# Kernel optimization log

Hardware: AMD Instinct MI355X
Metric: run time of the kernel (lower is better)

## Reference

```python
import jax, jax.numpy as jnp
import numpy as np

B, N, C, W = 128, 512, 128, 128
MASK_FILL = -1e-06  # faithful to original (sic: -1e-06, not -1e6)


def setup_inputs() -> dict:
    key = jax.random.key(0)
    ks = jax.random.split(key, 8)
    s = 1.0 / np.sqrt(C)
    return {
        "x": jax.random.normal(ks[0], (B, N, C), dtype=jnp.float32),
        "Wq": jax.random.normal(ks[1], (C, W), dtype=jnp.float32) * s,
        "bq": jnp.zeros((W,), dtype=jnp.float32),
        "Wk": jax.random.normal(ks[2], (C, W), dtype=jnp.float32) * s,
        "bk": jnp.zeros((W,), dtype=jnp.float32),
        "Wv": jax.random.normal(ks[3], (C, W), dtype=jnp.float32) * s,
        "bv": jnp.zeros((W,), dtype=jnp.float32),
        "valid_len": jax.random.randint(ks[4], (B,), 0, N, dtype=jnp.int64),
    }


def reference(x, Wq, bq, Wk, bk, Wv, bv, valid_len):
    # QKV projections: [B, N, W]
    q = jnp.einsum("bnc,cw->bnw", x, Wq) + bq
    k = jnp.einsum("bnc,cw->bnw", x, Wk) + bk
    v = jnp.einsum("bnc,cw->bnw", x, Wv) + bv
    # scores: [B, N, N]
    scores = jnp.einsum("bnw,bmw->bnm", q, k)
    # masked softmax: positions m where m > valid_len[b] get MASK_FILL
    # (mask is identical across query rows n since valid_len is per-batch)
    keep = jnp.arange(N)[None, None, :] <= valid_len[:, None, None]  # [B,1,N]
    scores = jnp.where(keep, scores, MASK_FILL)
    attn = jax.nn.softmax(scores, axis=-1)
    return jnp.einsum("bnm,bmw->bnw", attn, v)
```

## Files before the change

### kernel.cpp

```cpp
#include <hip/hip_runtime.h>
#include <hip/hip_fp16.h>

#define B_ 128
#define N_ 512
#define C_ 128
#define W_ 128
#define LDSW 136

typedef _Float16 f16;
typedef _Float16 f16x8 __attribute__((ext_vector_type(8)));
typedef _Float16 f16x4 __attribute__((ext_vector_type(4)));
typedef float f32x4 __attribute__((ext_vector_type(4)));

#define MFMA16(a, b, c) __builtin_amdgcn_mfma_f32_16x16x32_f16(a, b, c, 0, 0, 0)

__global__ __launch_bounds__(256) void prep_w(const float* __restrict__ Wq,
                                              const float* __restrict__ Wk,
                                              const float* __restrict__ Wv,
                                              f16* __restrict__ wT) {
  const float* src = blockIdx.x == 0 ? Wq : (blockIdx.x == 1 ? Wk : Wv);
  f16* dst = wT + (size_t)blockIdx.x * C_ * W_;
  const int t = threadIdx.x;
  for (int i = 0; i < 64; ++i) {
    int idx = t + 256 * i;
    int w = idx >> 7, c = idx & 127;
    dst[idx] = (f16)src[c * W_ + w];
  }
}

__global__ __launch_bounds__(256) void proj(const float* __restrict__ x,
                                            const float* __restrict__ bq,
                                            const float* __restrict__ bk,
                                            const float* __restrict__ bv,
                                            const f16* __restrict__ wT,
                                            f16* __restrict__ q,
                                            f16* __restrict__ k,
                                            f16* __restrict__ vT) {
  __shared__ f16 xs[128 * LDSW];
  __shared__ f16 wls[128 * LDSW];
  const int b = blockIdx.y, n0 = blockIdx.x * 128;
  const int t = threadIdx.x, wave = t >> 6, lane = t & 63;
  const int quad = lane >> 4, l15 = lane & 15;

  for (int i = 0; i < 16; ++i) {
    int idx = t + 256 * i;
    int row = idx >> 5, c4 = idx & 31;
    const float4 v = *reinterpret_cast<const float4*>(
        x + ((size_t)(b * N_ + n0 + row)) * C_ + c4 * 4);
    f16x4 h;
    h.x = (f16)v.x; h.y = (f16)v.y; h.z = (f16)v.z; h.w = (f16)v.w;
    *reinterpret_cast<f16x4*>(&xs[row * LDSW + c4 * 4]) = h;
  }
  __syncthreads();

  f16x8 af[2][4];
  for (int mt = 0; mt < 2; ++mt)
    for (int ks = 0; ks < 4; ++ks)
      af[mt][ks] = *reinterpret_cast<const f16x8*>(
          &xs[(wave * 32 + mt * 16 + l15) * LDSW + ks * 32 + quad * 8]);

  for (int ph = 0; ph < 3; ++ph) {
    __syncthreads();
    for (int i = 0; i < 8; ++i) {
      int idx = t + 256 * i;
      int row = idx >> 4, c16 = idx & 15;
      *reinterpret_cast<f16x8*>(&wls[row * LDSW + c16 * 8]) =
          *reinterpret_cast<const f16x8*>(wT + (size_t)ph * 16384 + idx * 8);
    }
    __syncthreads();

    f32x4 acc[2][8];
    for (int mt = 0; mt < 2; ++mt)
      for (int ct = 0; ct < 8; ++ct) acc[mt][ct] = {0.f, 0.f, 0.f, 0.f};

    for (int ct = 0; ct < 8; ++ct)
      for (int ks = 0; ks < 4; ++ks) {
        f16x8 bf = *reinterpret_cast<const f16x8*>(
            &wls[(ct * 16 + l15) * LDSW + ks * 32 + quad * 8]);
        acc[0][ct] = MFMA16(af[0][ks], bf, acc[0][ct]);
        acc[1][ct] = MFMA16(af[1][ks], bf, acc[1][ct]);
      }

    const float* bias = ph == 0 ? bq : (ph == 1 ? bk : bv);
    if (ph < 2) {
      f16* dst = ph == 0 ? q : k;
      for (int mt = 0; mt < 2; ++mt)
        for (int ct = 0; ct < 8; ++ct) {
          int wcol = ct * 16 + l15;
          float bb = bias[wcol];
          for (int r = 0; r < 4; ++r) {
            int n = n0 + wave * 32 + mt * 16 + quad * 4 + r;
            dst[((size_t)(b * N_ + n)) * W_ + wcol] = (f16)(acc[mt][ct][r] + bb);
          }
        }
    } else {
      for (int mt = 0; mt < 2; ++mt)
        for (int ct = 0; ct < 8; ++ct) {
          int wcol = ct * 16 + l15;
          float bb = bias[wcol];
          int n = n0 + wave * 32 + mt * 16 + quad * 4;
          f16x4 h;
          h.x = (f16)(acc[mt][ct][0] + bb);
          h.y = (f16)(acc[mt][ct][1] + bb);
          h.z = (f16)(acc[mt][ct][2] + bb);
          h.w = (f16)(acc[mt][ct][3] + bb);
          *reinterpret_cast<f16x4*>(&vT[((size_t)(b * W_ + wcol)) * N_ + n]) = h;
        }
    }
  }
}

__global__ __launch_bounds__(256, 2) void flash(const f16* __restrict__ q,
                                                const f16* __restrict__ k,
                                                const f16* __restrict__ vT,
                                                const int* __restrict__ vlen,
                                                float* __restrict__ out) {
  __shared__ f16 qls[128 * LDSW];
  __shared__ f16 pls[128 * LDSW];
  const int b = blockIdx.x, m0 = blockIdx.y * 128;
  const int t = threadIdx.x, wave = t >> 6, lane = t & 63;
  const int quad = lane >> 4, l15 = lane & 15;
  const int vl = vlen[b];

  for (int i = 0; i < 8; ++i) {
    int idx = t + 256 * i;
    int row = idx >> 4, c16 = idx & 15;
    *reinterpret_cast<f16x8*>(&qls[row * LDSW + c16 * 8]) =
        *reinterpret_cast<const f16x8*>(
            q + ((size_t)(b * N_ + m0 + row)) * W_ + c16 * 8);
  }
  __syncthreads();

  f32x4 oacc[2][8];
  for (int mt = 0; mt < 2; ++mt)
    for (int ct = 0; ct < 8; ++ct) oacc[mt][ct] = {0.f, 0.f, 0.f, 0.f};
  float mrun[8], lrun[8];
  for (int ct = 0; ct < 8; ++ct) { mrun[ct] = -3.4e38f; lrun[ct] = 0.f; }

  for (int j = 0; j < 4; ++j) {
    const int n0 = j * 128;

    f16x8 kf[2][4];
    for (int mt = 0; mt < 2; ++mt)
      for (int kt = 0; kt < 4; ++kt)
        kf[mt][kt] = *reinterpret_cast<const f16x8*>(
            k + ((size_t)(b * N_ + n0 + wave * 32 + mt * 16 + l15)) * W_ +
            kt * 32 + quad * 8);

    f32x4 sacc[2][8];
    for (int mt = 0; mt < 2; ++mt)
      for (int ct = 0; ct < 8; ++ct) sacc[mt][ct] = {0.f, 0.f, 0.f, 0.f};
    for (int ct = 0; ct < 8; ++ct)
      for (int kt = 0; kt < 4; ++kt) {
        f16x8 bf = *reinterpret_cast<const f16x8*>(
            &qls[(ct * 16 + l15) * LDSW + kt * 32 + quad * 8]);
        sacc[0][ct] = MFMA16(kf[0][kt], bf, sacc[0][ct]);
        sacc[1][ct] = MFMA16(kf[1][kt], bf, sacc[1][ct]);
      }

    for (int mt = 0; mt < 2; ++mt)
      for (int r = 0; r < 4; ++r) {
        int n = n0 + wave * 32 + mt * 16 + quad * 4 + r;
        if (n > vl)
          for (int ct = 0; ct < 8; ++ct) sacc[mt][ct][r] = -1e-6f;
      }

    float cm[8];
    for (int ct = 0; ct < 8; ++ct) {
      float c0 = fmaxf(fmaxf(sacc[0][ct][0], sacc[0][ct][1]),
                       fmaxf(sacc[0][ct][2], sacc[0][ct][3]));
      float c1 = fmaxf(fmaxf(sacc[1][ct][0], sacc[1][ct][1]),
                       fmaxf(sacc[1][ct][2], sacc[1][ct][3]));
      float c = fmaxf(c0, c1);
      c = fmaxf(c, __shfl_xor(c, 16));
      c = fmaxf(c, __shfl_xor(c, 32));
      cm[ct] = c;
    }
    __shared__ float redbuf[4 * 128];
    __syncthreads();
    if (quad == 0)
      for (int ct = 0; ct < 8; ++ct) redbuf[wave * 128 + ct * 16 + l15] = cm[ct];
    __syncthreads();
    float alpha[8];
    for (int ct = 0; ct < 8; ++ct) {
      int mcol = ct * 16 + l15;
      float c = fmaxf(fmaxf(redbuf[mcol], redbuf[128 + mcol]),
                      fmaxf(redbuf[256 + mcol], redbuf[384 + mcol]));
      float mnew = fmaxf(mrun[ct], c);
      alpha[ct] = __expf(mrun[ct] - mnew);
      mrun[ct] = mnew;
    }
    float ls[8];
    for (int ct = 0; ct < 8; ++ct) {
      float s = 0.f;
      for (int mt = 0; mt < 2; ++mt)
        for (int r = 0; r < 4; ++r) {
          float p = __expf(sacc[mt][ct][r] - mrun[ct]);
          sacc[mt][ct][r] = p;
          s += p;
        }
      s += __shfl_xor(s, 16);
      s += __shfl_xor(s, 32);
      ls[ct] = s;
    }
    if (quad == 0)
      for (int ct = 0; ct < 8; ++ct) redbuf[wave * 128 + ct * 16 + l15] = ls[ct];
    for (int mt = 0; mt < 2; ++mt)
      for (int ct = 0; ct < 8; ++ct) {
        f16x4 h;
        h.x = (f16)sacc[mt][ct][0];
        h.y = (f16)sacc[mt][ct][1];
        h.z = (f16)sacc[mt][ct][2];
        h.w = (f16)sacc[mt][ct][3];
        *reinterpret_cast<f16x4*>(
            &pls[(ct * 16 + l15) * LDSW + wave * 32 + mt * 16 + quad * 4]) = h;
      }
    f16x8 vf[2][4];
    for (int mt = 0; mt < 2; ++mt)
      for (int kt = 0; kt < 4; ++kt)
        vf[mt][kt] = *reinterpret_cast<const f16x8*>(
            vT + ((size_t)(b * W_ + wave * 32 + mt * 16 + l15)) * N_ + n0 +
            kt * 32 + quad * 8);
    __syncthreads();
    for (int ct = 0; ct < 8; ++ct) {
      int mcol = ct * 16 + l15;
      float s = redbuf[mcol] + redbuf[128 + mcol] + redbuf[256 + mcol] +
                redbuf[384 + mcol];
      lrun[ct] = lrun[ct] * alpha[ct] + s;
      oacc[0][ct] *= alpha[ct];
      oacc[1][ct] *= alpha[ct];
    }
    for (int ct = 0; ct < 8; ++ct)
      for (int kt = 0; kt < 4; ++kt) {
        f16x8 bf = *reinterpret_cast<const f16x8*>(
            &pls[(ct * 16 + l15) * LDSW + kt * 32 + quad * 8]);
        oacc[0][ct] = MFMA16(vf[0][kt], bf, oacc[0][ct]);
        oacc[1][ct] = MFMA16(vf[1][kt], bf, oacc[1][ct]);
      }
  }

  for (int ct = 0; ct < 8; ++ct) {
    float inv = 1.f / lrun[ct];
    int m = m0 + ct * 16 + l15;
    for (int mt = 0; mt < 2; ++mt) {
      int w = wave * 32 + mt * 16 + quad * 4;
      float4 o;
      o.x = oacc[mt][ct][0] * inv;
      o.y = oacc[mt][ct][1] * inv;
      o.z = oacc[mt][ct][2] * inv;
      o.w = oacc[mt][ct][3] * inv;
      *reinterpret_cast<float4*>(&out[((size_t)(b * N_ + m)) * W_ + w]) = o;
    }
  }
}

extern "C" void kernel_launch(void* const* d_in, const int* in_sizes, int n_in,
                              void* d_out, int out_size, void* d_ws,
                              size_t ws_size, hipStream_t stream) {
  const float* x  = (const float*)d_in[0];
  const float* Wq = (const float*)d_in[1];
  const float* bq = (const float*)d_in[2];
  const float* Wk = (const float*)d_in[3];
  const float* bk = (const float*)d_in[4];
  const float* Wv = (const float*)d_in[5];
  const float* bv = (const float*)d_in[6];
  const int* vlen = (const int*)d_in[7];
  float* out = (float*)d_out;

  char* ws = (char*)d_ws;
  f16* wT = (f16*)ws;
  f16* q  = (f16*)(ws + (1u << 20));
  f16* k  = (f16*)(ws + (1u << 20) + (16u << 20));
  f16* vT = (f16*)(ws + (1u << 20) + (32u << 20));

  prep_w<<<3, 256, 0, stream>>>(Wq, Wk, Wv, wT);
  proj<<<dim3(4, 128), 256, 0, stream>>>(x, bq, bk, bv, wT, q, k, vT);
  flash<<<dim3(128, 4), 256, 0, stream>>>(q, k, vT, vlen, out);
}
```

Before: 146.3 us.

## Give each wave its own query rows in flash to drop cross-wave softmax reductions

The flash kernel is restructured so each wave owns 32 query rows and covers all 128 keys per tile. Row max and row sum then reduce within the wave, which removes the shared-memory reduction buffer and most block-wide barriers. Q fragments stay in registers instead of LDS. Each wave now loads the whole K and V tile directly from global memory, so redundant global/L2 traffic goes up four times. Q is also pre-scaled by log2(e) in the projection so exp2f can replace __expf, and the weight transpose in prep_w now goes through LDS to get coalesced reads.

After: 172.5 us. 17.8% more time.

```diff
diff --git a/kernel.cpp b/kernel.cpp
--- a/kernel.cpp
+++ b/kernel.cpp
@@ -1,5 +1,6 @@
 #include <hip/hip_runtime.h>
 #include <hip/hip_fp16.h>
+#include <math.h>
 
 #define B_ 128
 #define N_ 512
@@ -14,17 +15,31 @@
 
 #define MFMA16(a, b, c) __builtin_amdgcn_mfma_f32_16x16x32_f16(a, b, c, 0, 0, 0)
 
+#define LOG2E 1.44269504f
+#define MASKF (-1e-6f * LOG2E)
+
 __global__ __launch_bounds__(256) void prep_w(const float* __restrict__ Wq,
                                               const float* __restrict__ Wk,
                                               const float* __restrict__ Wv,
                                               f16* __restrict__ wT) {
+  __shared__ float xs[128 * 129];
   const float* src = blockIdx.x == 0 ? Wq : (blockIdx.x == 1 ? Wk : Wv);
   f16* dst = wT + (size_t)blockIdx.x * C_ * W_;
   const int t = threadIdx.x;
+  for (int i = 0; i < 16; ++i) {
+    int idx = t + 256 * i;
+    int c = idx >> 5, w4 = idx & 31;
+    float4 v = *reinterpret_cast<const float4*>(src + c * W_ + w4 * 4);
+    xs[c * 129 + w4 * 4 + 0] = v.x;
+    xs[c * 129 + w4 * 4 + 1] = v.y;
+    xs[c * 129 + w4 * 4 + 2] = v.z;
+    xs[c * 129 + w4 * 4 + 3] = v.w;
+  }
+  __syncthreads();
   for (int i = 0; i < 64; ++i) {
     int idx = t + 256 * i;
     int w = idx >> 7, c = idx & 127;
-    dst[idx] = (f16)src[c * W_ + w];
+    dst[idx] = (f16)xs[c * 129 + w];
   }
 }
 
@@ -81,8 +96,9 @@
         acc[1][ct] = MFMA16(af[1][ks], bf, acc[1][ct]);
       }
 
-    const float* bias = ph == 0 ? bq : (ph == 1 ? bk : bv);
     if (ph < 2) {
+      const float* bias = ph == 0 ? bq : bk;
+      const float scale = ph == 0 ? LOG2E : 1.0f;
       f16* dst = ph == 0 ? q : k;
       for (int mt = 0; mt < 2; ++mt)
         for (int ct = 0; ct < 8; ++ct) {
@@ -90,14 +106,15 @@
           float bb = bias[wcol];
           for (int r = 0; r < 4; ++r) {
             int n = n0 + wave * 32 + mt * 16 + quad * 4 + r;
-            dst[((size_t)(b * N_ + n)) * W_ + wcol] = (f16)(acc[mt][ct][r] + bb);
+            dst[((size_t)(b * N_ + n)) * W_ + wcol] =
+                (f16)((acc[mt][ct][r] + bb) * scale);
           }
         }
     } else {
       for (int mt = 0; mt < 2; ++mt)
         for (int ct = 0; ct < 8; ++ct) {
           int wcol = ct * 16 + l15;
-          float bb = bias[wcol];
+          float bb = bv[wcol];
           int n = n0 + wave * 32 + mt * 16 + quad * 4;
           f16x4 h;
           h.x = (f16)(acc[mt][ct][0] + bb);
@@ -115,140 +132,118 @@
                                                 const f16* __restrict__ vT,
                                                 const int* __restrict__ vlen,
                                                 float* __restrict__ out) {
-  __shared__ f16 qls[128 * LDSW];
   __shared__ f16 pls[128 * LDSW];
   const int b = blockIdx.x, m0 = blockIdx.y * 128;
   const int t = threadIdx.x, wave = t >> 6, lane = t & 63;
   const int quad = lane >> 4, l15 = lane & 15;
   const int vl = vlen[b];
-
-  for (int i = 0; i < 8; ++i) {
-    int idx = t + 256 * i;
-    int row = idx >> 4, c16 = idx & 15;
-    *reinterpret_cast<f16x8*>(&qls[row * LDSW + c16 * 8]) =
-        *reinterpret_cast<const f16x8*>(
-            q + ((size_t)(b * N_ + m0 + row)) * W_ + c16 * 8);
-  }
-  __syncthreads();
-
-  f32x4 oacc[2][8];
-  for (int mt = 0; mt < 2; ++mt)
-    for (int ct = 0; ct < 8; ++ct) oacc[mt][ct] = {0.f, 0.f, 0.f, 0.f};
-  float mrun[8], lrun[8];
-  for (int ct = 0; ct < 8; ++ct) { mrun[ct] = -3.4e38f; lrun[ct] = 0.f; }
+  const int mcol = m0 + wave * 32;
+
+  f16x8 qf[2][4];
+  for (int ct = 0; ct < 2; ++ct)
+    for (int kt = 0; kt < 4; ++kt)
+      qf[ct][kt] = *reinterpret_cast<const f16x8*>(
+          q + ((size_t)(b * N_ + mcol + ct * 16 + l15)) * W_ + kt * 32 +
+          quad * 8);
+
+  f32x4 oacc[8][2];
+  for (int wt = 0; wt < 8; ++wt)
+    for (int ct = 0; ct < 2; ++ct) oacc[wt][ct] = {0.f, 0.f, 0.f, 0.f};
+  float mrun[2] = {-3.4e38f, -3.4e38f}, lrun[2] = {0.f, 0.f};
+
+  f16* prow = &pls[(size_t)wave * 32 * LDSW];
 
   for (int j = 0; j < 4; ++j) {
     const int n0 = j * 128;
 
-    f16x8 kf[2][4];
-    for (int mt = 0; mt < 2; ++mt)
+    f32x4 sacc[8][2];
+    for (int i = 0; i < 8; ++i) {
+      sacc[i][0] = {0.f, 0.f, 0.f, 0.f};
+      sacc[i][1] = {0.f, 0.f, 0.f, 0.f};
+      f16x8 kf[4];
       for (int kt = 0; kt < 4; ++kt)
-        kf[mt][kt] = *reinterpret_cast<const f16x8*>(
-            k + ((size_t)(b * N_ + n0 + wave * 32 + mt * 16 + l15)) * W_ +
-            kt * 32 + quad * 8);
-
-    f32x4 sacc[2][8];
-    for (int mt = 0; mt < 2; ++mt)
-      for (int ct = 0; ct < 8; ++ct) sacc[mt][ct] = {0.f, 0.f, 0.f, 0.f};
-    for (int ct = 0; ct < 8; ++ct)
+        kf[kt] = *reinterpret_cast<const f16x8*>(
+            k + ((size_t)(b * N_ + n0 + 16 * i + l15)) * W_ + kt * 32 +
+            quad * 8);
       for (int kt = 0; kt < 4; ++kt) {
-        f16x8 bf = *reinterpret_cast<const f16x8*>(
-            &qls[(ct * 16 + l15) * LDSW + kt * 32 + quad * 8]);
-        sacc[0][ct] = MFMA16(kf[0][kt], bf, sacc[0][ct]);
-        sacc[1][ct] = MFMA16(kf[1][kt], bf, sacc[1][ct]);
-      }
-
-    for (int mt = 0; mt < 2; ++mt)
+        sacc[i][0] = MFMA16(kf[kt], qf[0][kt], sacc[i][0]);
+        sacc[i][1] = MFMA16(kf[kt], qf[1][kt], sacc[i][1]);
+      }
+    }
+
+    for (int i = 0; i < 8; ++i)
       for (int r = 0; r < 4; ++r) {
-        int n = n0 + wave * 32 + mt * 16 + quad * 4 + r;
-        if (n > vl)
-          for (int ct = 0; ct < 8; ++ct) sacc[mt][ct][r] = -1e-6f;
-      }
-
-    float cm[8];
-    for (int ct = 0; ct < 8; ++ct) {
-      float c0 = fmaxf(fmaxf(sacc[0][ct][0], sacc[0][ct][1]),
-                       fmaxf(sacc[0][ct][2], sacc[0][ct][3]));
-      float c1 = fmaxf(fmaxf(sacc[1][ct][0], sacc[1][ct][1]),
-                       fmaxf(sacc[1][ct][2], sacc[1][ct][3]));
-      float c = fmaxf(c0, c1);
-      c = fmaxf(c, __shfl_xor(c, 16));
-      c = fmaxf(c, __shfl_xor(c, 32));
-      cm[ct] = c;
-    }
-    __shared__ float redbuf[4 * 128];
-    __syncthreads();
-    if (quad == 0)
-      for (int ct = 0; ct < 8; ++ct) redbuf[wave * 128 + ct * 16 + l15] = cm[ct];
-    __syncthreads();
-    float alpha[8];
-    for (int ct = 0; ct < 8; ++ct) {
-      int mcol = ct * 16 + l15;
-      float c = fmaxf(fmaxf(redbuf[mcol], redbuf[128 + mcol]),
-                      fmaxf(redbuf[256 + mcol], redbuf[384 + mcol]));
-      float mnew = fmaxf(mrun[ct], c);
-      alpha[ct] = __expf(mrun[ct] - mnew);
+        int n = n0 + 16 * i + quad * 4 + r;
+        if (n > vl) { sacc[i][0][r] = MASKF; sacc[i][1][r] = MASKF; }
+      }
+
+    float alpha[2];
+    for (int ct = 0; ct < 2; ++ct) {
+      float mx = -3.4e38f;
+      for (int i = 0; i < 8; ++i)
+        for (int r = 0; r < 4; ++r) mx = fmaxf(mx, sacc[i][ct][r]);
+      mx = fmaxf(mx, __shfl_xor(mx, 16));
+      mx = fmaxf(mx, __shfl_xor(mx, 32));
+      float mnew = fmaxf(mrun[ct], mx);
+      alpha[ct] = exp2f(mrun[ct] - mnew);
       mrun[ct] = mnew;
-    }
-    float ls[8];
-    for (int ct = 0; ct < 8; ++ct) {
       float s = 0.f;
-      for (int mt = 0; mt < 2; ++mt)
+      for (int i = 0; i < 8; ++i)
         for (int r = 0; r < 4; ++r) {
-          float p = __expf(sacc[mt][ct][r] - mrun[ct]);
-          sacc[mt][ct][r] = p;
+          float p = exp2f(sacc[i][ct][r] - mnew);
+          sacc[i][ct][r] = p;
           s += p;
         }
       s += __shfl_xor(s, 16);
       s += __shfl_xor(s, 32);
-      ls[ct] = s;
-    }
-    if (quad == 0)
-      for (int ct = 0; ct < 8; ++ct) redbuf[wave * 128 + ct * 16 + l15] = ls[ct];
-    for (int mt = 0; mt < 2; ++mt)
-      for (int ct = 0; ct < 8; ++ct) {
+      lrun[ct] = lrun[ct] * alpha[ct] + s;
+    }
+
+    for (int i = 0; i < 8; ++i)
+      for (int ct = 0; ct < 2; ++ct) {
         f16x4 h;
-        h.x = (f16)sacc[mt][ct][0];
-        h.y = (f16)sacc[mt][ct][1];
-        h.z = (f16)sacc[mt][ct][2];
-        h.w = (f16)sacc[mt][ct][3];
+        h.x = (f16)sacc[i][ct][0];
+        h.y = (f16)sacc[i][ct][1];
+        h.z = (f16)sacc[i][ct][2];
+        h.w = (f16)sacc[i][ct][3];
         *reinterpret_cast<f16x4*>(
-            &pls[(ct * 16 + l15) * LDSW + wave * 32 + mt * 16 + quad * 4]) = h;
-      }
-    f16x8 vf[2][4];
-    for (int mt = 0; mt < 2; ++mt)
+            &prow[(ct * 16 + l15) * LDSW + 16 * i + quad * 4]) = h;
+      }
+
+    for (int wt = 0; wt < 8; ++wt) {
+      oacc[wt][0] *= alpha[0];
+      oacc[wt][1] *= alpha[1];
+    }
+
+    f16x8 pf[2][4];
+    for (int ct = 0; ct < 2; ++ct)
       for (int kt = 0; kt < 4; ++kt)
-        vf[mt][kt] = *reinterpret_cast<const f16x8*>(
-            vT + ((size_t)(b * W_ + wave * 32 + mt * 16 + l15)) * N_ + n0 +
-            kt * 32 + quad * 8);
-    __syncthreads();
-    for (int ct = 0; ct < 8; ++ct) {
-      int mcol = ct * 16 + l15;
-      float s = redbuf[mcol] + redbuf[128 + mcol] + redbuf[256 + mcol] +
-                redbuf[384 + mcol];
-      lrun[ct] = lrun[ct] * alpha[ct] + s;
-      oacc[0][ct] *= alpha[ct];
-      oacc[1][ct] *= alpha[ct];
-    }
-    for (int ct = 0; ct < 8; ++ct)
+        pf[ct][kt] = *reinterpret_cast<const f16x8*>(
+            &prow[(ct * 16 + l15) * LDSW + kt * 32 + quad * 8]);
+
+    for (int wt = 0; wt < 8; ++wt) {
+      f16x8 vf[4];
+      for (int kt = 0; kt < 4; ++kt)
+        vf[kt] = *reinterpret_cast<const f16x8*>(
+            vT + ((size_t)(b * W_ + 16 * wt + l15)) * N_ + n0 + kt * 32 +
+            quad * 8);
       for (int kt = 0; kt < 4; ++kt) {
-        f16x8 bf = *reinterpret_cast<const f16x8*>(
-            &pls[(ct * 16 + l15) * LDSW + kt * 32 + quad * 8]);
-        oacc[0][ct] = MFMA16(vf[0][kt], bf, oacc[0][ct]);
-        oacc[1][ct] = MFMA16(vf[1][kt], bf, oacc[1][ct]);
-      }
-  }
-
-  for (int ct = 0; ct < 8; ++ct) {
+        oacc[wt][0] = MFMA16(vf[kt], pf[0][kt], oacc[wt][0]);
+        oacc[wt][1] = MFMA16(vf[kt], pf[1][kt], oacc[wt][1]);
+      }
+    }
+  }
+
+  for (int ct = 0; ct < 2; ++ct) {
     float inv = 1.f / lrun[ct];
-    int m = m0 + ct * 16 + l15;
-    for (int mt = 0; mt < 2; ++mt) {
-      int w = wave * 32 + mt * 16 + quad * 4;
+    int m = mcol + ct * 16 + l15;
+    for (int wt = 0; wt < 8; ++wt) {
+      int w = 16 * wt + quad * 4;
       float4 o;
-      o.x = oacc[mt][ct][0] * inv;
-      o.y = oacc[mt][ct][1] * inv;
-      o.z = oacc[mt][ct][2] * inv;
-      o.w = oacc[mt][ct][3] * inv;
+      o.x = oacc[wt][ct][0] * inv;
+      o.y = oacc[wt][ct][1] * inv;
+      o.z = oacc[wt][ct][2] * inv;
+      o.w = oacc[wt][ct][3] * inv;
       *reinterpret_cast<float4*>(&out[((size_t)(b * N_ + m)) * W_ + w]) = o;
     }
   }
```
